# Optimization experiments

Hardware: AMD Instinct MI355X
Metric: run time of the kernel (lower is better)

## Reference

```python
import jax, jax.numpy as jnp
import numpy as np

EMBED_DIM = 1024
NUM_HEADS = 16
HEAD_DIM = EMBED_DIM // NUM_HEADS


def setup_inputs() -> dict:
    key = jax.random.key(0)
    k_x, k_wqkv, k_bqkv, k_wp, k_bp = jax.random.split(key, 5)
    B, S = 4, 2048
    scale = 1.0 / np.sqrt(EMBED_DIM)
    return {
        "x": jax.random.normal(k_x, (B, S, EMBED_DIM), dtype=jnp.float32),
        "w_qkv": jax.random.uniform(k_wqkv, (EMBED_DIM, 3 * EMBED_DIM), jnp.float32, -scale, scale),
        "b_qkv": jax.random.uniform(k_bqkv, (3 * EMBED_DIM,), jnp.float32, -scale, scale),
        "w_proj": jax.random.uniform(k_wp, (EMBED_DIM, EMBED_DIM), jnp.float32, -scale, scale),
        "b_proj": jax.random.uniform(k_bp, (EMBED_DIM,), jnp.float32, -scale, scale),
    }


def reference(x, w_qkv, b_qkv, w_proj, b_proj):
    B, S, E = x.shape
    H, D = NUM_HEADS, HEAD_DIM
    # fused QKV projection: [B,S,3E] -> [3,B,H,S,D]
    qkv = (x @ w_qkv + b_qkv).reshape(B, S, 3, H, D).transpose(2, 0, 3, 1, 4)
    q, k, v = qkv[0], qkv[1], qkv[2]
    scores = jnp.einsum("bhqd,bhkd->bhqk", q, k) / np.sqrt(D).astype(jnp.float32)
    attn = jax.nn.softmax(scores, axis=-1)  # dropout is identity in eval
    out = jnp.einsum("bhqk,bhkd->bhqd", attn, v)
    out = out.transpose(0, 2, 1, 3).reshape(B, S, E)
    return out @ w_proj + b_proj
```

## Files before the change

### kernel.cpp

```cpp
#include <hip/hip_runtime.h>
#include <hip/hip_bf16.h>

#define PB 4
#define PS 2048
#define PH 16
#define PD 64
#define PE 1024

typedef short v8s __attribute__((ext_vector_type(8)));
typedef float v4f __attribute__((ext_vector_type(4)));

#define QSCALE 0.18033688f

__device__ __forceinline__ ushort f2b(float f) {
  union { __hip_bfloat16 b; ushort u; } cv;
  cv.b = __float2bfloat16(f);
  return cv.u;
}

#if __has_builtin(__builtin_amdgcn_exp2f)
__device__ __forceinline__ float fexp2(float x) { return __builtin_amdgcn_exp2f(x); }
#else
__device__ __forceinline__ float fexp2(float x) { return exp2f(x); }
#endif

__device__ __forceinline__ void cp16(const __hip_bfloat16* g, __hip_bfloat16* l) {
  __builtin_amdgcn_global_load_lds(
      (const __attribute__((address_space(1))) void*)g,
      (__attribute__((address_space(3))) void*)l, 16, 0, 0);
}

__global__ __launch_bounds__(256) void conv_f2b(const float* __restrict__ S,
                                                __hip_bfloat16* __restrict__ D) {
  int i = blockIdx.x * 256 + threadIdx.x;
  float4 f = reinterpret_cast<const float4*>(S)[i];
  union { ushort u[4]; uint2 v; } pk;
  pk.u[0] = f2b(f.x); pk.u[1] = f2b(f.y); pk.u[2] = f2b(f.z); pk.u[3] = f2b(f.w);
  reinterpret_cast<uint2*>(D)[i] = pk.v;
}

__global__ __launch_bounds__(256) void transp_f2b(const float* __restrict__ S,
                                                  __hip_bfloat16* __restrict__ D,
                                                  int R, int C) {
  __shared__ float tile[32][33];
  const int t = threadIdx.x;
  const int tx = t & 31, ty = t >> 5;
  const int r0 = blockIdx.y * 32, c0 = blockIdx.x * 32;
#pragma unroll
  for (int i = 0; i < 4; ++i)
    tile[ty + 8 * i][tx] = S[(size_t)(r0 + ty + 8 * i) * C + c0 + tx];
  __syncthreads();
#pragma unroll
  for (int i = 0; i < 4; ++i)
    D[(size_t)(c0 + ty + 8 * i) * R + r0 + tx] = __float2bfloat16(tile[tx][ty + 8 * i]);
}

template <int MODE>
__global__ __launch_bounds__(256) void gemm_bt(
    const __hip_bfloat16* __restrict__ A, const __hip_bfloat16* __restrict__ BT,
    const float* __restrict__ bias, void* __restrict__ outv) {
  __shared__ __hip_bfloat16 As[128 * 64];
  __shared__ __hip_bfloat16 Bs[128 * 64];
  const int t = threadIdx.x;
  const int lane = t & 63, w = t >> 6;
  const int ln = lane & 15, qd = lane >> 4;
  const int wm = w >> 1, wn = w & 1;
  const int m0 = blockIdx.y * 128, n0 = blockIdx.x * 128;
  v4f acc[4][4] = {};

  for (int k0 = 0; k0 < PE; k0 += 64) {
    __syncthreads();
#pragma unroll
    for (int i = 0; i < 4; ++i) {
      int idx = t + 256 * i;
      int r = idx >> 3, cs = idx & 7;
      int cg = cs ^ (r & 7);
      cp16(A + (size_t)(m0 + r) * PE + k0 + cg * 8, As + idx * 8);
      cp16(BT + (size_t)(n0 + r) * PE + k0 + cg * 8, Bs + idx * 8);
    }
    __syncthreads();
#pragma unroll
    for (int kk = 0; kk < 2; ++kk) {
      v8s af[4], bf[4];
#pragma unroll
      for (int mb = 0; mb < 4; ++mb) {
        int ra = wm * 64 + mb * 16 + ln;
        int ca = (kk * 4 + qd) ^ (ra & 7);
        af[mb] = *reinterpret_cast<const v8s*>(As + ra * 64 + ca * 8);
      }
#pragma unroll
      for (int nb = 0; nb < 4; ++nb) {
        int rb = wn * 64 + nb * 16 + ln;
        int cb = (kk * 4 + qd) ^ (rb & 7);
        bf[nb] = *reinterpret_cast<const v8s*>(Bs + rb * 64 + cb * 8);
      }
#pragma unroll
      for (int mb = 0; mb < 4; ++mb)
#pragma unroll
        for (int nb = 0; nb < 4; ++nb)
          acc[mb][nb] = __builtin_amdgcn_mfma_f32_16x16x32_bf16(af[mb], bf[nb],
                                                                acc[mb][nb], 0, 0, 0);
    }
  }

  const int mwb = m0 + wm * 64 + qd * 4;
  const int nwb = n0 + wn * 64 + ln;
  if (MODE == 0) {
    __hip_bfloat16* QKV = (__hip_bfloat16*)outv;
#pragma unroll
    for (int nb = 0; nb < 4; ++nb) {
      int n = nwb + nb * 16;
      float bv = bias[n];
      int which = n >> 10, h = (n >> 6) & 15, d = n & 63;
#pragma unroll
      for (int mb = 0; mb < 4; ++mb) {
        int r0 = mwb + mb * 16;
        int b = r0 >> 11, s0 = r0 & (PS - 1);
        v4f a = acc[mb][nb];
        if (which == 2) {
          union { ushort u[4]; uint2 v; } pk;
#pragma unroll
          for (int i = 0; i < 4; ++i) pk.u[i] = f2b(a[i] + bv);
          size_t idx = (((size_t)(2 * PB + b) * PH + h) * PD + d) * PS + s0;
          *reinterpret_cast<uint2*>(&QKV[idx]) = pk.v;
        } else {
          float sc = (which == 0) ? QSCALE : 1.0f;
          size_t base = (((size_t)(which * PB + b) * PH + h) * PS + s0) * PD + d;
#pragma unroll
          for (int i = 0; i < 4; ++i)
            QKV[base + (size_t)i * PD] = __float2bfloat16((a[i] + bv) * sc);
        }
      }
    }
  } else {
    float* Co = (float*)outv;
#pragma unroll
    for (int nb = 0; nb < 4; ++nb) {
      int n = nwb + nb * 16;
      float bv = bias[n];
#pragma unroll
      for (int mb = 0; mb < 4; ++mb) {
        int r0 = mwb + mb * 16;
        v4f a = acc[mb][nb];
#pragma unroll
        for (int i = 0; i < 4; ++i)
          Co[(size_t)(r0 + i) * PE + n] = a[i] + bv;
      }
    }
  }
}

__global__ __launch_bounds__(256) void attn_mfma4(
    const __hip_bfloat16* __restrict__ QKV, __hip_bfloat16* __restrict__ O) {
  __shared__ __hip_bfloat16 Ks[128 * 64];
  __shared__ __hip_bfloat16 Vts[64 * 128];
  const int t = threadIdx.x;
  const int lane = t & 63, w = t >> 6;
  const int ln = lane & 15, qd = lane >> 4;
  const int b = blockIdx.y >> 4, h = blockIdx.y & 15;
  const int q0 = blockIdx.x * 128;
  const __hip_bfloat16* Qb = QKV + (size_t)(b * PH + h) * PS * PD;
  const __hip_bfloat16* Kb = QKV + (size_t)((PB + b) * PH + h) * PS * PD;
  const __hip_bfloat16* Vb = QKV + (size_t)((2 * PB + b) * PH + h) * PD * PS;

  v8s qf[2][2];
#pragma unroll
  for (int u = 0; u < 2; ++u) {
    size_t qr = (size_t)(q0 + 32 * w + 16 * u + ln) * PD;
    qf[u][0] = *reinterpret_cast<const v8s*>(Qb + qr + qd * 8);
    qf[u][1] = *reinterpret_cast<const v8s*>(Qb + qr + 32 + qd * 8);
  }
  v4f oacc[2][4] = {};
  float lrow[2] = {0.f, 0.f};

  for (int kt = 0; kt < PS; kt += 128) {
    __syncthreads();
#pragma unroll
    for (int i = 0; i < 4; ++i) {
      int idx = t + 256 * i;
      int rk = idx >> 3, ck = (idx & 7) ^ (rk & 7);
      cp16(Kb + (size_t)(kt + rk) * PD + ck * 8, Ks + idx * 8);
      int rv = idx >> 4, cv = (idx & 15) ^ (rv & 7);
      cp16(Vb + (size_t)rv * PS + kt + cv * 8, Vts + idx * 8);
    }
    __syncthreads();

    uint2 pw[2][8];
#pragma unroll
    for (int u = 0; u < 2; ++u) {
      float psum = 0.f;
#pragma unroll
      for (int nb = 0; nb < 8; ++nb) {
        int nr = nb * 16 + ln;
        int c0 = qd ^ (nr & 7);
        v8s k0 = *reinterpret_cast<const v8s*>(Ks + nr * 64 + c0 * 8);
        v8s k1 = *reinterpret_cast<const v8s*>(Ks + nr * 64 + (c0 ^ 4) * 8);
        v4f z = {};
        z = __builtin_amdgcn_mfma_f32_16x16x32_bf16(k0, qf[u][0], z, 0, 0, 0);
        v4f sv = __builtin_amdgcn_mfma_f32_16x16x32_bf16(k1, qf[u][1], z, 0, 0, 0);
        union { ushort pu[4]; uint2 pv; } pk;
#pragma unroll
        for (int i = 0; i < 4; ++i) {
          float p = fexp2(sv[i]);
          psum += p;
          pk.pu[i] = f2b(p);
        }
        pw[u][nb] = pk.pv;
      }
      psum += __shfl_xor(psum, 16);
      psum += __shfl_xor(psum, 32);
      lrow[u] += psum;
    }

#pragma unroll
    for (int s = 0; s < 4; ++s) {
      union { v8s v; uint2 u2[2]; } a0, a1;
      a0.u2[0] = pw[0][2 * s]; a0.u2[1] = pw[0][2 * s + 1];
      a1.u2[0] = pw[1][2 * s]; a1.u2[1] = pw[1][2 * s + 1];
#pragma unroll
      for (int db = 0; db < 4; ++db) {
        int rv = db * 16 + ln;
        const uint2* vrow = reinterpret_cast<const uint2*>(Vts + rv * 128);
        int L0 = 4 * s + (qd >> 1);
        union { v8s v; uint2 u2[2]; } vf;
        vf.u2[0] = vrow[((L0 ^ (rv & 7)) << 1) | (qd & 1)];
        vf.u2[1] = vrow[(((L0 + 2) ^ (rv & 7)) << 1) | (qd & 1)];
        oacc[0][db] = __builtin_amdgcn_mfma_f32_16x16x32_bf16(a0.v, vf.v,
                                                              oacc[0][db], 0, 0, 0);
        oacc[1][db] = __builtin_amdgcn_mfma_f32_16x16x32_bf16(a1.v, vf.v,
                                                              oacc[1][db], 0, 0, 0);
      }
    }
  }
#pragma unroll
  for (int u = 0; u < 2; ++u) {
#pragma unroll
    for (int i = 0; i < 4; ++i) {
      float inv = 1.f / __shfl(lrow[u], qd * 4 + i);
      int sg = q0 + 32 * w + 16 * u + qd * 4 + i;
      size_t base = (((size_t)b * PS + sg) * PH + h) * PD;
#pragma unroll
      for (int db = 0; db < 4; ++db)
        O[base + db * 16 + ln] = __float2bfloat16(oacc[u][db][i] * inv);
    }
  }
}

__device__ __forceinline__ uint2 load4bf(const float* p) {
  const float4 f = *reinterpret_cast<const float4*>(p);
  union { ushort u[4]; uint2 v; } pk;
  pk.u[0] = f2b(f.x); pk.u[1] = f2b(f.y); pk.u[2] = f2b(f.z); pk.u[3] = f2b(f.w);
  return pk.v;
}
__device__ __forceinline__ uint2 load4bf(const __hip_bfloat16* p) {
  return *reinterpret_cast<const uint2*>(p);
}

template <typename AT, int MODE>
__global__ __launch_bounds__(256) void gemm128(
    const AT* __restrict__ A, const float* __restrict__ Bm,
    const float* __restrict__ bias, void* __restrict__ outv, int ldb) {
  __shared__ __hip_bfloat16 As[128][40];
  __shared__ __hip_bfloat16 Bs[128][40];
  const int t = threadIdx.x;
  const int lane = t & 63, w = t >> 6;
  const int ln = lane & 15, qd = lane >> 4;
  const int wm = w >> 1, wn = w & 1;
  const int m0 = blockIdx.y * 128, n0 = blockIdx.x * 128;
  v4f acc[4][4] = {};
  for (int k0 = 0; k0 < PE; k0 += 32) {
    __syncthreads();
#pragma unroll
    for (int i = 0; i < 4; ++i) {
      int p = t + 256 * i;
      int m = p >> 3, kc = p & 7;
      *reinterpret_cast<uint2*>(&As[m][kc * 4]) =
          load4bf(A + (size_t)(m0 + m) * PE + k0 + kc * 4);
    }
#pragma unroll
    for (int i = 0; i < 4; ++i) {
      int p = t + 256 * i;
      int n = p & 127, kc = p >> 7;
      union { ushort u[4]; uint2 v; } pk;
#pragma unroll
      for (int r = 0; r < 4; ++r)
        pk.u[r] = f2b(Bm[(size_t)(k0 + kc * 4 + r) * ldb + n0 + n]);
      *reinterpret_cast<uint2*>(&Bs[n][kc * 4]) = pk.v;
    }
    __syncthreads();
    v8s af[4], bf[4];
#pragma unroll
    for (int mb = 0; mb < 4; ++mb)
      af[mb] = *reinterpret_cast<const v8s*>(&As[wm * 64 + mb * 16 + ln][qd * 8]);
#pragma unroll
    for (int nb = 0; nb < 4; ++nb)
      bf[nb] = *reinterpret_cast<const v8s*>(&Bs[wn * 64 + nb * 16 + ln][qd * 8]);
#pragma unroll
    for (int mb = 0; mb < 4; ++mb)
#pragma unroll
      for (int nb = 0; nb < 4; ++nb)
        acc[mb][nb] = __builtin_amdgcn_mfma_f32_16x16x32_bf16(af[mb], bf[nb],
                                                              acc[mb][nb], 0, 0, 0);
  }
  const int mwb = m0 + wm * 64 + qd * 4;
  const int nwb = n0 + wn * 64 + ln;
  if (MODE == 0) {
    __hip_bfloat16* QKV = (__hip_bfloat16*)outv;
#pragma unroll
    for (int nb = 0; nb < 4; ++nb) {
      int n = nwb + nb * 16;
      float bv = bias[n];
      int which = n >> 10, h = (n >> 6) & 15, d = n & 63;
#pragma unroll
      for (int mb = 0; mb < 4; ++mb) {
        int r0 = mwb + mb * 16;
        int b = r0 >> 11, s0 = r0 & (PS - 1);
        v4f a = acc[mb][nb];
        if (which == 2) {
          union { ushort u[4]; uint2 v; } pk;
#pragma unroll
          for (int i = 0; i < 4; ++i) pk.u[i] = f2b(a[i] + bv);
          size_t idx = (((size_t)(2 * PB + b) * PH + h) * PD + d) * PS + s0;
          *reinterpret_cast<uint2*>(&QKV[idx]) = pk.v;
        } else {
          float sc = (which == 0) ? QSCALE : 1.0f;
          size_t base = (((size_t)(which * PB + b) * PH + h) * PS + s0) * PD + d;
#pragma unroll
          for (int i = 0; i < 4; ++i)
            QKV[base + (size_t)i * PD] = __float2bfloat16((a[i] + bv) * sc);
        }
      }
    }
  } else {
    float* Co = (float*)outv;
#pragma unroll
    for (int nb = 0; nb < 4; ++nb) {
      int n = nwb + nb * 16;
      float bv = bias[n];
#pragma unroll
      for (int mb = 0; mb < 4; ++mb) {
        int r0 = mwb + mb * 16;
        v4f a = acc[mb][nb];
#pragma unroll
        for (int i = 0; i < 4; ++i)
          Co[(size_t)(r0 + i) * PE + n] = a[i] + bv;
      }
    }
  }
}

extern "C" void kernel_launch(void* const* d_in, const int* in_sizes, int n_in,
                              void* d_out, int out_size, void* d_ws,
                              size_t ws_size, hipStream_t stream) {
  const float* x = (const float*)d_in[0];
  const float* w_qkv = (const float*)d_in[1];
  const float* b_qkv = (const float*)d_in[2];
  const float* w_proj = (const float*)d_in[3];
  const float* b_proj = (const float*)d_in[4];
  float* out = (float*)d_out;

  const size_t xE = (size_t)PB * PS * PE;
  const size_t wqE = (size_t)PE * 3 * PE;
  const size_t wpE = (size_t)PE * PE;
  const size_t qkvE = (size_t)3 * PB * PH * PS * PD;
  const size_t needMain = (xE + wqE + wpE + qkvE) * 2;

  dim3 blk(256);
  dim3 gq(24, 64), ga(16, 64), gp(8, 64);

  if (ws_size >= needMain) {
    __hip_bfloat16* xb = (__hip_bfloat16*)d_ws;
    __hip_bfloat16* wqkvT = xb + xE;
    __hip_bfloat16* wprojT = wqkvT + wqE;
    __hip_bfloat16* qkv = wprojT + wpE;
    __hip_bfloat16* o = xb;

    conv_f2b<<<dim3(xE / 1024), blk, 0, stream>>>(x, xb);
    transp_f2b<<<dim3(96, 32), blk, 0, stream>>>(w_qkv, wqkvT, PE, 3 * PE);
    transp_f2b<<<dim3(32, 32), blk, 0, stream>>>(w_proj, wprojT, PE, PE);
    gemm_bt<0><<<gq, blk, 0, stream>>>(xb, wqkvT, b_qkv, qkv);
    attn_mfma4<<<ga, blk, 0, stream>>>(qkv, o);
    gemm_bt<1><<<gp, blk, 0, stream>>>(o, wprojT, b_proj, out);
  } else {
    __hip_bfloat16* qkv = (__hip_bfloat16*)d_ws;
    if (ws_size >= (qkvE + xE) * 2) {
      __hip_bfloat16* o = qkv + qkvE;
      gemm128<float, 0><<<gq, blk, 0, stream>>>(x, w_qkv, b_qkv, qkv, 3 * PE);
      attn_mfma4<<<ga, blk, 0, stream>>>(qkv, o);
      gemm128<__hip_bfloat16, 1><<<gp, blk, 0, stream>>>(o, w_proj, b_proj, out, PE);
    } else {
      __hip_bfloat16* o = (__hip_bfloat16*)d_out;
      float* tmp = (float*)d_ws;
      gemm128<float, 0><<<gq, blk, 0, stream>>>(x, w_qkv, b_qkv, qkv, 3 * PE);
      attn_mfma4<<<ga, blk, 0, stream>>>(qkv, o);
      gemm128<__hip_bfloat16, 1><<<gp, blk, 0, stream>>>(o, w_proj, b_proj, tmp, PE);
      hipMemcpyAsync(d_out, tmp, xE * sizeof(float), hipMemcpyDeviceToDevice, stream);
    }
  }
}
```

Measured before the change: 286.9 us.

## Double-buffer K/V tiles in attention with async LDS loads and manual waitcnt

The attention kernel now keeps two LDS buffers for K and V^T tiles. It issues the global-to-LDS copies for the next tile before computing on the current one, using explicit vmcnt waits and raw s_barrier in place of __syncthreads, so load latency overlaps with MFMA work. It also raises wave priority around the PV MFMA loop and precomputes the swizzled LDS offsets. LDS use doubles to 64KB per block, which may reduce occupancy, and the hand-written waitcnt counts must match the number of outstanding loads exactly.

```diff
diff --git a/kernel.cpp b/kernel.cpp
--- a/kernel.cpp
+++ b/kernel.cpp
@@ -28,6 +28,12 @@
   __builtin_amdgcn_global_load_lds(
       (const __attribute__((address_space(1))) void*)g,
       (__attribute__((address_space(3))) void*)l, 16, 0, 0);
+}
+
+__device__ __forceinline__ void barrier_fence() {
+  asm volatile("" ::: "memory");
+  __builtin_amdgcn_s_barrier();
+  asm volatile("" ::: "memory");
 }
 
 __global__ __launch_bounds__(256) void conv_f2b(const float* __restrict__ S,
@@ -150,10 +156,10 @@
   }
 }
 
-__global__ __launch_bounds__(256) void attn_mfma4(
+__global__ __launch_bounds__(256) void attn_mfma5(
     const __hip_bfloat16* __restrict__ QKV, __hip_bfloat16* __restrict__ O) {
-  __shared__ __hip_bfloat16 Ks[128 * 64];
-  __shared__ __hip_bfloat16 Vts[64 * 128];
+  __shared__ __hip_bfloat16 Ks[2][128 * 64];
+  __shared__ __hip_bfloat16 Vts[2][64 * 128];
   const int t = threadIdx.x;
   const int lane = t & 63, w = t >> 6;
   const int ln = lane & 15, qd = lane >> 4;
@@ -173,28 +179,43 @@
   v4f oacc[2][4] = {};
   float lrow[2] = {0.f, 0.f};
 
-  for (int kt = 0; kt < PS; kt += 128) {
-    __syncthreads();
+  const int r7 = ln & 7;
+  const int c0 = qd ^ r7;
+  const int q1 = qd & 1, qh = qd >> 1;
+  int soff[4][2];
+#pragma unroll
+  for (int s = 0; s < 4; ++s) {
+    int L0 = 4 * s + qh;
+    soff[s][0] = (((L0 ^ r7) << 1) | q1);
+    soff[s][1] = ((((L0 + 2) ^ r7) << 1) | q1);
+  }
+  int rvoff[4];
+#pragma unroll
+  for (int db = 0; db < 4; ++db) rvoff[db] = (db * 16 + ln) * 32;
+
+  auto STAGE = [&](int buf, int kt) {
 #pragma unroll
     for (int i = 0; i < 4; ++i) {
       int idx = t + 256 * i;
       int rk = idx >> 3, ck = (idx & 7) ^ (rk & 7);
-      cp16(Kb + (size_t)(kt + rk) * PD + ck * 8, Ks + idx * 8);
+      cp16(Kb + (size_t)(kt + rk) * PD + ck * 8, Ks[buf] + idx * 8);
       int rv = idx >> 4, cv = (idx & 15) ^ (rv & 7);
-      cp16(Vb + (size_t)rv * PS + kt + cv * 8, Vts + idx * 8);
-    }
-    __syncthreads();
-
+      cp16(Vb + (size_t)rv * PS + kt + cv * 8, Vts[buf] + idx * 8);
+    }
+  };
+
+  auto COMPUTE = [&](int buf) {
+    const __hip_bfloat16* Kbuf = Ks[buf];
+    const uint2* Vbuf = reinterpret_cast<const uint2*>(Vts[buf]);
     uint2 pw[2][8];
 #pragma unroll
     for (int u = 0; u < 2; ++u) {
       float psum = 0.f;
 #pragma unroll
       for (int nb = 0; nb < 8; ++nb) {
-        int nr = nb * 16 + ln;
-        int c0 = qd ^ (nr & 7);
-        v8s k0 = *reinterpret_cast<const v8s*>(Ks + nr * 64 + c0 * 8);
-        v8s k1 = *reinterpret_cast<const v8s*>(Ks + nr * 64 + (c0 ^ 4) * 8);
+        const __hip_bfloat16* kr = Kbuf + (nb * 16 + ln) * 64;
+        v8s k0 = *reinterpret_cast<const v8s*>(kr + c0 * 8);
+        v8s k1 = *reinterpret_cast<const v8s*>(kr + (c0 ^ 4) * 8);
         v4f z = {};
         z = __builtin_amdgcn_mfma_f32_16x16x32_bf16(k0, qf[u][0], z, 0, 0, 0);
         v4f sv = __builtin_amdgcn_mfma_f32_16x16x32_bf16(k1, qf[u][1], z, 0, 0, 0);
@@ -211,27 +232,45 @@
       psum += __shfl_xor(psum, 32);
       lrow[u] += psum;
     }
-
 #pragma unroll
     for (int s = 0; s < 4; ++s) {
       union { v8s v; uint2 u2[2]; } a0, a1;
       a0.u2[0] = pw[0][2 * s]; a0.u2[1] = pw[0][2 * s + 1];
       a1.u2[0] = pw[1][2 * s]; a1.u2[1] = pw[1][2 * s + 1];
+      __builtin_amdgcn_s_setprio(1);
 #pragma unroll
       for (int db = 0; db < 4; ++db) {
-        int rv = db * 16 + ln;
-        const uint2* vrow = reinterpret_cast<const uint2*>(Vts + rv * 128);
-        int L0 = 4 * s + (qd >> 1);
         union { v8s v; uint2 u2[2]; } vf;
-        vf.u2[0] = vrow[((L0 ^ (rv & 7)) << 1) | (qd & 1)];
-        vf.u2[1] = vrow[(((L0 + 2) ^ (rv & 7)) << 1) | (qd & 1)];
+        vf.u2[0] = Vbuf[rvoff[db] + soff[s][0]];
+        vf.u2[1] = Vbuf[rvoff[db] + soff[s][1]];
         oacc[0][db] = __builtin_amdgcn_mfma_f32_16x16x32_bf16(a0.v, vf.v,
                                                               oacc[0][db], 0, 0, 0);
         oacc[1][db] = __builtin_amdgcn_mfma_f32_16x16x32_bf16(a1.v, vf.v,
                                                               oacc[1][db], 0, 0, 0);
       }
-    }
-  }
+      __builtin_amdgcn_s_setprio(0);
+    }
+  };
+
+  STAGE(0, 0);
+#pragma unroll 1
+  for (int it = 0; it < PS / 128; it += 2) {
+    STAGE(1, (it + 1) * 128);
+    asm volatile("s_waitcnt vmcnt(8)" ::: "memory");
+    barrier_fence();
+    COMPUTE(0);
+    barrier_fence();
+    if (it + 2 < PS / 128) {
+      STAGE(0, (it + 2) * 128);
+      asm volatile("s_waitcnt vmcnt(8)" ::: "memory");
+    } else {
+      asm volatile("s_waitcnt vmcnt(0)" ::: "memory");
+    }
+    barrier_fence();
+    COMPUTE(1);
+    barrier_fence();
+  }
+
 #pragma unroll
   for (int u = 0; u < 2; ++u) {
 #pragma unroll
@@ -379,20 +418,20 @@
     transp_f2b<<<dim3(96, 32), blk, 0, stream>>>(w_qkv, wqkvT, PE, 3 * PE);
     transp_f2b<<<dim3(32, 32), blk, 0, stream>>>(w_proj, wprojT, PE, PE);
     gemm_bt<0><<<gq, blk, 0, stream>>>(xb, wqkvT, b_qkv, qkv);
-    attn_mfma4<<<ga, blk, 0, stream>>>(qkv, o);
+    attn_mfma5<<<ga, blk, 0, stream>>>(qkv, o);
     gemm_bt<1><<<gp, blk, 0, stream>>>(o, wprojT, b_proj, out);
   } else {
     __hip_bfloat16* qkv = (__hip_bfloat16*)d_ws;
     if (ws_size >= (qkvE + xE) * 2) {
       __hip_bfloat16* o = qkv + qkvE;
       gemm128<float, 0><<<gq, blk, 0, stream>>>(x, w_qkv, b_qkv, qkv, 3 * PE);
-      attn_mfma4<<<ga, blk, 0, stream>>>(qkv, o);
+      attn_mfma5<<<ga, blk, 0, stream>>>(qkv, o);
       gemm128<__hip_bfloat16, 1><<<gp, blk, 0, stream>>>(o, w_proj, b_proj, out, PE);
     } else {
       __hip_bfloat16* o = (__hip_bfloat16*)d_out;
       float* tmp = (float*)d_ws;
       gemm128<float, 0><<<gq, blk, 0, stream>>>(x, w_qkv, b_qkv, qkv, 3 * PE);
-      attn_mfma4<<<ga, blk, 0, stream>>>(qkv, o);
+      attn_mfma5<<<ga, blk, 0, stream>>>(qkv, o);
       gemm128<__hip_bfloat16, 1><<<gp, blk, 0, stream>>>(o, w_proj, b_proj, tmp, PE);
       hipMemcpyAsync(d_out, tmp, xE * sizeof(float), hipMemcpyDeviceToDevice, stream);
     }
```

New measurement: 318.4 us. 11.0% more time.

## Load attention K/V directly from global memory and add XCD-aware block swizzle

Applied to the files above, without the earlier changes.

The attention kernel drops its shared-memory K/V staging and block barriers. Each wave now loads its K and V fragments straight from global memory in 64-key steps, and s_setprio is raised around the PV MFMAs. Both GEMM and attention blocks are remapped so neighbouring tiles land on the same XCD, which should improve L2 reuse. The cost is redundant global/L2 traffic, because all four waves in a block fetch the same K/V data.

```diff
diff --git a/kernel.cpp b/kernel.cpp
--- a/kernel.cpp
+++ b/kernel.cpp
@@ -28,6 +28,10 @@
   __builtin_amdgcn_global_load_lds(
       (const __attribute__((address_space(1))) void*)g,
       (__attribute__((address_space(3))) void*)l, 16, 0, 0);
+}
+
+__device__ __forceinline__ int xcd_swz(int orig, int nwg) {
+  return (orig & 7) * (nwg >> 3) + (orig >> 3);
 }
 
 __global__ __launch_bounds__(256) void conv_f2b(const float* __restrict__ S,
@@ -65,7 +69,9 @@
   const int lane = t & 63, w = t >> 6;
   const int ln = lane & 15, qd = lane >> 4;
   const int wm = w >> 1, wn = w & 1;
-  const int m0 = blockIdx.y * 128, n0 = blockIdx.x * 128;
+  const int gx = gridDim.x;
+  const int swz = xcd_swz(blockIdx.y * gx + blockIdx.x, gx * gridDim.y);
+  const int m0 = (swz / gx) * 128, n0 = (swz % gx) * 128;
   v4f acc[4][4] = {};
 
   for (int k0 = 0; k0 < PE; k0 += 64) {
@@ -150,15 +156,15 @@
   }
 }
 
-__global__ __launch_bounds__(256) void attn_mfma4(
+__global__ __launch_bounds__(256) void attn_mfma12(
     const __hip_bfloat16* __restrict__ QKV, __hip_bfloat16* __restrict__ O) {
-  __shared__ __hip_bfloat16 Ks[128 * 64];
-  __shared__ __hip_bfloat16 Vts[64 * 128];
   const int t = threadIdx.x;
   const int lane = t & 63, w = t >> 6;
   const int ln = lane & 15, qd = lane >> 4;
-  const int b = blockIdx.y >> 4, h = blockIdx.y & 15;
-  const int q0 = blockIdx.x * 128;
+  const int swz = xcd_swz(blockIdx.y * 16 + blockIdx.x, 16 * 64);
+  const int bx = swz & 15, by = swz >> 4;
+  const int b = by >> 4, h = by & 15;
+  const int q0 = bx * 128;
   const __hip_bfloat16* Qb = QKV + (size_t)(b * PH + h) * PS * PD;
   const __hip_bfloat16* Kb = QKV + (size_t)((PB + b) * PH + h) * PS * PD;
   const __hip_bfloat16* Vb = QKV + (size_t)((2 * PB + b) * PH + h) * PD * PS;
@@ -173,31 +179,27 @@
   v4f oacc[2][4] = {};
   float lrow[2] = {0.f, 0.f};
 
-  for (int kt = 0; kt < PS; kt += 128) {
-    __syncthreads();
-#pragma unroll
-    for (int i = 0; i < 4; ++i) {
-      int idx = t + 256 * i;
-      int rk = idx >> 3, ck = (idx & 7) ^ (rk & 7);
-      cp16(Kb + (size_t)(kt + rk) * PD + ck * 8, Ks + idx * 8);
-      int rv = idx >> 4, cv = (idx & 15) ^ (rv & 7);
-      cp16(Vb + (size_t)rv * PS + kt + cv * 8, Vts + idx * 8);
-    }
-    __syncthreads();
-
-    uint2 pw[2][8];
+  const __hip_bfloat16* kp = Kb + (size_t)ln * PD + qd * 8;
+  const __hip_bfloat16* vp = Vb + (size_t)ln * PS + qd * 4;
+
+#pragma unroll 1
+  for (int kt = 0; kt < PS; kt += 64) {
+    v8s kf0[4], kf1[4];
+#pragma unroll
+    for (int nb = 0; nb < 4; ++nb) {
+      const __hip_bfloat16* kr = kp + (size_t)(kt + nb * 16) * PD;
+      kf0[nb] = *reinterpret_cast<const v8s*>(kr);
+      kf1[nb] = *reinterpret_cast<const v8s*>(kr + 32);
+    }
+    uint2 pw[2][4];
 #pragma unroll
     for (int u = 0; u < 2; ++u) {
       float psum = 0.f;
 #pragma unroll
-      for (int nb = 0; nb < 8; ++nb) {
-        int nr = nb * 16 + ln;
-        int c0 = qd ^ (nr & 7);
-        v8s k0 = *reinterpret_cast<const v8s*>(Ks + nr * 64 + c0 * 8);
-        v8s k1 = *reinterpret_cast<const v8s*>(Ks + nr * 64 + (c0 ^ 4) * 8);
+      for (int nb = 0; nb < 4; ++nb) {
         v4f z = {};
-        z = __builtin_amdgcn_mfma_f32_16x16x32_bf16(k0, qf[u][0], z, 0, 0, 0);
-        v4f sv = __builtin_amdgcn_mfma_f32_16x16x32_bf16(k1, qf[u][1], z, 0, 0, 0);
+        z = __builtin_amdgcn_mfma_f32_16x16x32_bf16(kf0[nb], qf[u][0], z, 0, 0, 0);
+        v4f sv = __builtin_amdgcn_mfma_f32_16x16x32_bf16(kf1[nb], qf[u][1], z, 0, 0, 0);
         union { ushort pu[4]; uint2 pv; } pk;
 #pragma unroll
         for (int i = 0; i < 4; ++i) {
@@ -211,27 +213,27 @@
       psum += __shfl_xor(psum, 32);
       lrow[u] += psum;
     }
-
-#pragma unroll
-    for (int s = 0; s < 4; ++s) {
+#pragma unroll
+    for (int s = 0; s < 2; ++s) {
       union { v8s v; uint2 u2[2]; } a0, a1;
       a0.u2[0] = pw[0][2 * s]; a0.u2[1] = pw[0][2 * s + 1];
       a1.u2[0] = pw[1][2 * s]; a1.u2[1] = pw[1][2 * s + 1];
+      __builtin_amdgcn_s_setprio(1);
 #pragma unroll
       for (int db = 0; db < 4; ++db) {
-        int rv = db * 16 + ln;
-        const uint2* vrow = reinterpret_cast<const uint2*>(Vts + rv * 128);
-        int L0 = 4 * s + (qd >> 1);
+        const __hip_bfloat16* vr = vp + (size_t)(db * 16) * PS + kt + s * 32;
         union { v8s v; uint2 u2[2]; } vf;
-        vf.u2[0] = vrow[((L0 ^ (rv & 7)) << 1) | (qd & 1)];
-        vf.u2[1] = vrow[(((L0 + 2) ^ (rv & 7)) << 1) | (qd & 1)];
+        vf.u2[0] = *reinterpret_cast<const uint2*>(vr);
+        vf.u2[1] = *reinterpret_cast<const uint2*>(vr + 16);
         oacc[0][db] = __builtin_amdgcn_mfma_f32_16x16x32_bf16(a0.v, vf.v,
                                                               oacc[0][db], 0, 0, 0);
         oacc[1][db] = __builtin_amdgcn_mfma_f32_16x16x32_bf16(a1.v, vf.v,
                                                               oacc[1][db], 0, 0, 0);
       }
-    }
-  }
+      __builtin_amdgcn_s_setprio(0);
+    }
+  }
+
 #pragma unroll
   for (int u = 0; u < 2; ++u) {
 #pragma unroll
@@ -379,20 +381,20 @@
     transp_f2b<<<dim3(96, 32), blk, 0, stream>>>(w_qkv, wqkvT, PE, 3 * PE);
     transp_f2b<<<dim3(32, 32), blk, 0, stream>>>(w_proj, wprojT, PE, PE);
     gemm_bt<0><<<gq, blk, 0, stream>>>(xb, wqkvT, b_qkv, qkv);
-    attn_mfma4<<<ga, blk, 0, stream>>>(qkv, o);
+    attn_mfma12<<<ga, blk, 0, stream>>>(qkv, o);
     gemm_bt<1><<<gp, blk, 0, stream>>>(o, wprojT, b_proj, out);
   } else {
     __hip_bfloat16* qkv = (__hip_bfloat16*)d_ws;
     if (ws_size >= (qkvE + xE) * 2) {
       __hip_bfloat16* o = qkv + qkvE;
       gemm128<float, 0><<<gq, blk, 0, stream>>>(x, w_qkv, b_qkv, qkv, 3 * PE);
-      attn_mfma4<<<ga, blk, 0, stream>>>(qkv, o);
+      attn_mfma12<<<ga, blk, 0, stream>>>(qkv, o);
       gemm128<__hip_bfloat16, 1><<<gp, blk, 0, stream>>>(o, w_proj, b_proj, out, PE);
     } else {
       __hip_bfloat16* o = (__hip_bfloat16*)d_out;
       float* tmp = (float*)d_ws;
       gemm128<float, 0><<<gq, blk, 0, stream>>>(x, w_qkv, b_qkv, qkv, 3 * PE);
-      attn_mfma4<<<ga, blk, 0, stream>>>(qkv, o);
+      attn_mfma12<<<ga, blk, 0, stream>>>(qkv, o);
       gemm128<__hip_bfloat16, 1><<<gp, blk, 0, stream>>>(o, w_proj, b_proj, tmp, PE);
       hipMemcpyAsync(d_out, tmp, xE * sizeof(float), hipMemcpyDeviceToDevice, stream);
     }
```

Result: slower. 528.3 us (+84.1%).
